# Kernel optimization log

Measured on AMD Instinct MI355X. Metric: run time of the kernel, lower is better.

## Reference

```python
import jax, jax.numpy as jnp
import numpy as np

FP4_VALUES = jnp.array([0.0, 0.5, 1.0, 1.5, 2.0, 3.0, 4.0, 6.0,
                        -0.0, -0.5, -1.0, -1.5, -2.0, -3.0, -4.0, -6.0], dtype=jnp.float32)
ALPHA = 1.702   # swiglu alpha
LIMIT = 7.0     # swiglu clamp limit
TOP_K = 4       # experts per token
EPS = 1e-5      # rmsnorm eps


def dequant_mxfp4(blocks, scales):
    """blocks: [E, R, G, B] int (uint8 values), scales: [E, R, G] int (E8M0 biased exp).
    Returns decoded weights [E, R, G*2B] fp32. Low nibble -> even cols, high nibble -> odd."""
    lo = FP4_VALUES[blocks & 15]
    hi = FP4_VALUES[(blocks >> 4) & 15]
    vals = jnp.stack([lo, hi], axis=-1).reshape(blocks.shape[:-1] + (-1,))  # [E,R,G,2B]
    w = jnp.ldexp(vals, (scales - 127)[..., None])
    return w.reshape(blocks.shape[:-2] + (-1,))


def rmsnorm(x, w):
    return x * jax.lax.rsqrt(jnp.mean(x * x, axis=-1, keepdims=True) + EPS) * w


def setup_inputs():
    key = jax.random.key(0)
    ks = jax.random.split(key, 10)
    E, H, I, B, S = 32, 1024, 1024, 1, 1024
    GB = 16  # packed bytes per 32-element group
    return {
        "x": jax.random.normal(ks[0], (B, S, H), jnp.float32),
        "norm_w": jnp.ones((H,), jnp.float32),
        "gate_w": jax.random.normal(ks[1], (E, H), jnp.float32) * 0.05,
        "gate_b": jax.random.normal(ks[2], (E,), jnp.float32) * 0.01,
        "mlp1_bias": jax.random.normal(ks[3], (E, 2 * I), jnp.float32) * 0.02,
        "mlp2_bias": jax.random.normal(ks[4], (E, H), jnp.float32) * 0.02,
        "mlp1_blocks": jax.random.randint(ks[5], (E, 2 * I, H // 32, GB), 0, 256, jnp.int32),
        "mlp1_scales": jax.random.randint(ks[6], (E, 2 * I, H // 32), 118, 125, jnp.int32),
        "mlp2_blocks": jax.random.randint(ks[7], (E, H, I // 32, GB), 0, 256, jnp.int32),
        "mlp2_scales": jax.random.randint(ks[8], (E, H, I // 32), 118, 125, jnp.int32),
    }


def reference(x, norm_w, gate_w, gate_b, mlp1_bias, mlp2_bias,
              mlp1_blocks, mlp1_scales, mlp2_blocks, mlp2_scales):
    B, S, H = x.shape
    N = B * S
    E = gate_w.shape[0]

    t = rmsnorm(x, norm_w).reshape(N, H)
    logits = t @ gate_w.T + gate_b                      # [N, E]
    top_vals, top_idx = jax.lax.top_k(logits, TOP_K)     # sorted descending, like torch.topk
    top_w = jax.nn.softmax(top_vals, axis=-1)            # [N, K]
    # dense routing matrix: nonzero only at selected experts (indices unique per token)
    route = jnp.zeros((N, E), x.dtype).at[jnp.arange(N)[:, None], top_idx].add(top_w)

    w1 = dequant_mxfp4(mlp1_blocks, mlp1_scales)         # [E, 2I, H]
    w2 = dequant_mxfp4(mlp2_blocks, mlp2_scales)         # [E, H, I]

    h = jnp.einsum('nh,eih->nei', t, w1) + mlp1_bias[None]  # [N, E, 2I]
    x_glu = jnp.minimum(h[..., 0::2], LIMIT)
    x_lin = jnp.clip(h[..., 1::2], -LIMIT, LIMIT)
    a = x_glu * jax.nn.sigmoid(ALPHA * x_glu) * (x_lin + 1.0)   # [N, E, I]
    y = jnp.einsum('nei,ehi->neh', a, w2) + mlp2_bias[None]      # [N, E, H]
    out = jnp.einsum('neh,ne->nh', y, route)                     # weighted combine
    return x + out.reshape(B, S, H)
```

## Files before the change

kernel.cpp:

```cpp
#include <hip/hip_runtime.h>
#include <hip/hip_bf16.h>
#include <math.h>


#define NE 32
#define HD 1024
#define ID 1024
#define NTOK 1024
#define R1 2048
#define TCH 160

typedef __attribute__((ext_vector_type(8)))  short bf16x8;
typedef __attribute__((ext_vector_type(16))) float f32x16;

#define TB_OFF   0
#define A_OFF    2097152
#define YB_OFF   10485760
#define CNT_OFF  18874368
#define OFFS_OFF 18874624
#define TOKL_OFF 18874880
#define TIDX_OFF 19005952
#define TWT_OFF  19022336
#define POS_OFF  19038720

__device__ __forceinline__ unsigned f2bf(float f) {
    unsigned u = __float_as_uint(f);
    return (u + 0x7FFFu + ((u >> 16) & 1u)) >> 16;
}
__device__ __forceinline__ float bf2f(unsigned u) {
    return __uint_as_float(u << 16);
}

__device__ __forceinline__ void dec8(int4 wv, unsigned dd, uint4& o) {
    unsigned u = __builtin_amdgcn_perm((unsigned)wv.y, (unsigned)wv.x, 0x00000400u);
    unsigned v = __builtin_amdgcn_perm((unsigned)wv.w, (unsigned)wv.z, 0x04000000u);
    unsigned packed = __builtin_amdgcn_perm(v, u, 0x07060100u);
    unsigned selE = packed & 0x07070707u;
    unsigned sE   = packed & 0x08080808u;
    unsigned ph   = packed >> 4;
    unsigned selO = ph & 0x07070707u;
    unsigned sO   = ph & 0x08080808u;
    const unsigned PH_hi = 0x40404040u, PH_lo = 0x3F3F3F14u;
    const unsigned PL_hi = 0xC0804000u, PL_lo = 0xC0800000u;
    unsigned hbE = __builtin_amdgcn_perm(PH_hi, PH_lo, selE) | (sE << 4);
    unsigned lbE = __builtin_amdgcn_perm(PL_hi, PL_lo, selE);
    unsigned hbO = __builtin_amdgcn_perm(PH_hi, PH_lo, selO) | (sO << 4);
    unsigned lbO = __builtin_amdgcn_perm(PL_hi, PL_lo, selO);
    unsigned mE0 = __builtin_amdgcn_perm(hbE, lbE, 0x05010400u);
    unsigned mE1 = __builtin_amdgcn_perm(hbE, lbE, 0x07030602u);
    unsigned mO0 = __builtin_amdgcn_perm(hbO, lbO, 0x05010400u);
    unsigned mO1 = __builtin_amdgcn_perm(hbO, lbO, 0x07030602u);
    unsigned r0 = __builtin_amdgcn_perm(mO0, mE0, 0x05040100u);
    unsigned r1 = __builtin_amdgcn_perm(mO0, mE0, 0x07060302u);
    unsigned r2 = __builtin_amdgcn_perm(mO1, mE1, 0x05040100u);
    unsigned r3 = __builtin_amdgcn_perm(mO1, mE1, 0x07060302u);
    unsigned o0, o1, o2, o3;
    asm("v_pk_add_u16 %0, %1, %2" : "=v"(o0) : "v"(r0), "v"(dd));
    asm("v_pk_add_u16 %0, %1, %2" : "=v"(o1) : "v"(r1), "v"(dd));
    asm("v_pk_add_u16 %0, %1, %2" : "=v"(o2) : "v"(r2), "v"(dd));
    asm("v_pk_add_u16 %0, %1, %2" : "=v"(o3) : "v"(r3), "v"(dd));
    o.x = o0; o.y = o1; o.z = o2; o.w = o3;
}

__global__ __launch_bounds__(256) void k_gate(
    const float* __restrict__ x, const float* __restrict__ norm_w,
    const float* __restrict__ gate_w, const float* __restrict__ gate_b,
    ushort* __restrict__ t_bf16, int* __restrict__ top_idx, float* __restrict__ top_wt)
{
    int n = blockIdx.x;
    int tid = threadIdx.x;
    __shared__ float tl[HD];
    __shared__ float red[4];
    __shared__ float logits[NE];

    const float4* xv = (const float4*)(x + (size_t)n * HD);
    float4 v = xv[tid];
    float ss = v.x * v.x + v.y * v.y + v.z * v.z + v.w * v.w;
    #pragma unroll
    for (int off = 32; off; off >>= 1) ss += __shfl_down(ss, off);
    if ((tid & 63) == 0) red[tid >> 6] = ss;
    __syncthreads();
    float tot = red[0] + red[1] + red[2] + red[3];
    float rms = rsqrtf(tot * (1.0f / HD) + 1e-5f);

    float4 w = ((const float4*)norm_w)[tid];
    float4 tv;
    tv.x = v.x * rms * w.x; tv.y = v.y * rms * w.y;
    tv.z = v.z * rms * w.z; tv.w = v.w * rms * w.w;
    ushort4 tb;
    tb.x = (ushort)f2bf(tv.x); tb.y = (ushort)f2bf(tv.y);
    tb.z = (ushort)f2bf(tv.z); tb.w = (ushort)f2bf(tv.w);
    ((ushort4*)(t_bf16 + (size_t)n * HD))[tid] = tb;
    ((float4*)tl)[tid] = tv;
    __syncthreads();

    int wv = tid >> 6, lane = tid & 63;
    for (int j = 0; j < 8; j++) {
        int e = wv * 8 + j;
        const float* gw = gate_w + (size_t)e * HD;
        float p = 0.f;
        #pragma unroll
        for (int q = 0; q < 16; q++) { int kk = lane + q * 64; p += tl[kk] * gw[kk]; }
        #pragma unroll
        for (int off = 32; off; off >>= 1) p += __shfl_down(p, off);
        if (lane == 0) logits[e] = p + gate_b[e];
    }
    __syncthreads();

    if (tid == 0) {
        float vals[4]; int idx[4];
        unsigned used = 0;
        #pragma unroll
        for (int kk = 0; kk < 4; kk++) {
            float best = -1e30f; int bi = 0;
            for (int e2 = 0; e2 < NE; e2++) {
                if (used & (1u << e2)) continue;
                if (logits[e2] > best) { best = logits[e2]; bi = e2; }
            }
            used |= 1u << bi; vals[kk] = best; idx[kk] = bi;
        }
        float m = vals[0], s = 0.f, ex[4];
        #pragma unroll
        for (int kk = 0; kk < 4; kk++) { ex[kk] = __expf(vals[kk] - m); s += ex[kk]; }
        float inv = 1.0f / s;
        #pragma unroll
        for (int kk = 0; kk < 4; kk++) {
            top_idx[n * 4 + kk] = idx[kk];
            top_wt[n * 4 + kk] = ex[kk] * inv;
        }
    }
}

__global__ void k_build(const int* __restrict__ top_idx, int* __restrict__ counts,
                        int* __restrict__ tok_list, int* __restrict__ pos_of)
{
    int i = blockIdx.x * 256 + threadIdx.x;
    if (i >= NTOK * 4) return;
    int n = i >> 2;
    int e = top_idx[i];
    int slot = atomicAdd(counts + e, 1);
    tok_list[e * NTOK + slot] = n;
    pos_of[i] = slot;
}

__global__ void k_prefix(const int* __restrict__ counts, int* __restrict__ offsets)
{
    if (threadIdx.x == 0) {
        int s = 0;
        for (int e = 0; e < NE; e++) { offsets[e] = s; s += counts[e]; }
        offsets[NE] = s;
    }
}

__global__ __launch_bounds__(256) void k_mlp1(
    const ushort* __restrict__ t_bf16, const int* __restrict__ blocks,
    const int* __restrict__ scales, const float* __restrict__ bias,
    const int* __restrict__ counts, const int* __restrict__ offsets,
    const int* __restrict__ tok_list, ushort* __restrict__ a)
{
    int e = blockIdx.y;
    int cnt = counts[e];
    if (cnt == 0) return;
    int r0 = blockIdx.x * 128;
    int tid = threadIdx.x;
    int w = tid >> 6, l = tid & 63;
    int base = offsets[e];

    __shared__ ushort tl[TCH][72];
    __shared__ ushort wl[128][72];
    __shared__ int tlist[TCH];

    int lrow = r0 + w * 32 + (l & 31);
    float b_lane = bias[e * R1 + lrow];
    int srow = tid >> 1, shalf = tid & 1;

    for (int c0 = 0; c0 < cnt; c0 += TCH) {
        int nt = min(TCH, cnt - c0);
        __syncthreads();
        if (tid < TCH) tlist[tid] = tok_list[e * NTOK + c0 + min(tid, nt - 1)];
        f32x16 acc[5] = {};

        #pragma unroll 1
        for (int k0 = 0; k0 < HD; k0 += 64) {
            __syncthreads();
            for (int idx = tid; idx < TCH * 8; idx += 256) {
                int tok = idx >> 3, seg = idx & 7;
                *(uint4*)&tl[tok][seg * 8] =
                    *(const uint4*)(t_bf16 + (size_t)tlist[tok] * HD + k0 + seg * 8);
            }
            {
                int g = (k0 >> 5) + shalf;
                size_t rbase = (size_t)(e * R1 + r0 + srow) * 32 + g;
                int s = scales[rbase];
                unsigned dd16 = (unsigned)((s - 127) << 7) & 0xFFFFu;
                unsigned dd = dd16 | (dd16 << 16);
                const int4* wp = (const int4*)(blocks + rbase * 16);
                ushort* dst = &wl[srow][shalf * 32];
                #pragma unroll
                for (int q = 0; q < 4; q++) {
                    uint4 ov;
                    dec8(wp[q], dd, ov);
                    *(uint4*)(dst + q * 8) = ov;
                }
            }
            __syncthreads();
            #pragma unroll
            for (int ks = 0; ks < 4; ks++) {
                bf16x8 wf = *(const bf16x8*)&wl[w * 32 + (l & 31)][ks * 16 + (l >> 5) * 8];
                #pragma unroll
                for (int mt = 0; mt < 5; mt++) {
                    bf16x8 af = *(const bf16x8*)&tl[mt * 32 + (l & 31)][ks * 16 + (l >> 5) * 8];
                    acc[mt] = __builtin_amdgcn_mfma_f32_32x32x16_bf16(af, wf, acc[mt], 0, 0, 0);
                }
            }
        }

        int p0 = (r0 + w * 32) >> 1;
        int pcol = p0 + ((l & 31) >> 1);
        #pragma unroll
        for (int mt = 0; mt < 5; mt++) {
            #pragma unroll
            for (int r = 0; r < 16; r++) {
                float h = acc[mt][r] + b_lane;
                float other = __shfl_xor(h, 1, 64);
                int m = (r & 3) + 8 * (r >> 2) + 4 * (l >> 5);
                int tokg = c0 + mt * 32 + m;
                if (!(l & 1) && tokg < cnt) {
                    float hg = fminf(h, 7.0f);
                    float hx = fminf(fmaxf(other, -7.0f), 7.0f);
                    float sig = 1.0f / (1.0f + __expf(-1.702f * hg));
                    float av = hg * sig * (hx + 1.0f);
                    a[(size_t)(base + tokg) * ID + pcol] = (ushort)f2bf(av);
                }
            }
        }
    }
}

__global__ __launch_bounds__(256) void k_mlp2(
    const ushort* __restrict__ a, const int* __restrict__ blocks,
    const int* __restrict__ scales, const float* __restrict__ bias,
    const int* __restrict__ counts, const int* __restrict__ offsets,
    ushort* __restrict__ yb)
{
    int e = blockIdx.y;
    int cnt = counts[e];
    if (cnt == 0) return;
    int r0 = blockIdx.x * 128;
    int tid = threadIdx.x;
    int w = tid >> 6, l = tid & 63;
    int base = offsets[e];

    __shared__ ushort tl[TCH][72];
    __shared__ ushort wl[128][72];

    int lrow = r0 + w * 32 + (l & 31);
    float b_lane = bias[e * HD + lrow];
    int srow = tid >> 1, shalf = tid & 1;

    for (int c0 = 0; c0 < cnt; c0 += TCH) {
        int nt = min(TCH, cnt - c0);
        f32x16 acc[5] = {};

        #pragma unroll 1
        for (int k0 = 0; k0 < ID; k0 += 64) {
            __syncthreads();
            for (int idx = tid; idx < TCH * 8; idx += 256) {
                int tok = idx >> 3, seg = idx & 7;
                int slot = base + c0 + min(tok, nt - 1);
                *(uint4*)&tl[tok][seg * 8] =
                    *(const uint4*)(a + (size_t)slot * ID + k0 + seg * 8);
            }
            {
                int g = (k0 >> 5) + shalf;
                size_t rbase = (size_t)(e * HD + r0 + srow) * 32 + g;
                int s = scales[rbase];
                unsigned dd16 = (unsigned)((s - 127) << 7) & 0xFFFFu;
                unsigned dd = dd16 | (dd16 << 16);
                const int4* wp = (const int4*)(blocks + rbase * 16);
                ushort* dst = &wl[srow][shalf * 32];
                #pragma unroll
                for (int q = 0; q < 4; q++) {
                    uint4 ov;
                    dec8(wp[q], dd, ov);
                    *(uint4*)(dst + q * 8) = ov;
                }
            }
            __syncthreads();
            #pragma unroll
            for (int ks = 0; ks < 4; ks++) {
                bf16x8 wf = *(const bf16x8*)&wl[w * 32 + (l & 31)][ks * 16 + (l >> 5) * 8];
                #pragma unroll
                for (int mt = 0; mt < 5; mt++) {
                    bf16x8 af = *(const bf16x8*)&tl[mt * 32 + (l & 31)][ks * 16 + (l >> 5) * 8];
                    acc[mt] = __builtin_amdgcn_mfma_f32_32x32x16_bf16(af, wf, acc[mt], 0, 0, 0);
                }
            }
        }

        int hcol = r0 + w * 32 + (l & 31);
        #pragma unroll
        for (int mt = 0; mt < 5; mt++) {
            #pragma unroll
            for (int r = 0; r < 16; r++) {
                int m = (r & 3) + 8 * (r >> 2) + 4 * (l >> 5);
                int tokg = c0 + mt * 32 + m;
                if (tokg < cnt) {
                    float y = acc[mt][r] + b_lane;
                    yb[(size_t)(base + tokg) * HD + hcol] = (ushort)f2bf(y);
                }
            }
        }
    }
}

__global__ __launch_bounds__(256) void k_combine(
    const float* __restrict__ x, const ushort* __restrict__ yb,
    const int* __restrict__ top_idx, const float* __restrict__ top_wt,
    const int* __restrict__ pos_of, const int* __restrict__ offsets,
    float* __restrict__ out)
{
    int n = blockIdx.x, tid = threadIdx.x;
    float4 xv = ((const float4*)(x + (size_t)n * HD))[tid];
    float r0 = xv.x, r1 = xv.y, r2 = xv.z, r3 = xv.w;
    #pragma unroll
    for (int k = 0; k < 4; k++) {
        int e = top_idx[n * 4 + k];
        float wt = top_wt[n * 4 + k];
        int slot = offsets[e] + pos_of[n * 4 + k];
        ushort4 yv = ((const ushort4*)(yb + (size_t)slot * HD))[tid];
        r0 += wt * bf2f(yv.x); r1 += wt * bf2f(yv.y);
        r2 += wt * bf2f(yv.z); r3 += wt * bf2f(yv.w);
    }
    float4 ov; ov.x = r0; ov.y = r1; ov.z = r2; ov.w = r3;
    ((float4*)(out + (size_t)n * HD))[tid] = ov;
}

extern "C" void kernel_launch(void* const* d_in, const int* in_sizes, int n_in,
                              void* d_out, int out_size, void* d_ws, size_t ws_size,
                              hipStream_t stream)
{
    const float* x           = (const float*)d_in[0];
    const float* norm_w      = (const float*)d_in[1];
    const float* gate_w      = (const float*)d_in[2];
    const float* gate_b      = (const float*)d_in[3];
    const float* mlp1_bias   = (const float*)d_in[4];
    const float* mlp2_bias   = (const float*)d_in[5];
    const int*   mlp1_blocks = (const int*)d_in[6];
    const int*   mlp1_scales = (const int*)d_in[7];
    const int*   mlp2_blocks = (const int*)d_in[8];
    const int*   mlp2_scales = (const int*)d_in[9];
    float* out = (float*)d_out;

    char* ws = (char*)d_ws;
    ushort* t_bf16  = (ushort*)(ws + TB_OFF);
    ushort* a       = (ushort*)(ws + A_OFF);
    ushort* yb      = (ushort*)(ws + YB_OFF);
    int*   counts   = (int*)(ws + CNT_OFF);
    int*   offsets  = (int*)(ws + OFFS_OFF);
    int*   tok_list = (int*)(ws + TOKL_OFF);
    int*   top_idx  = (int*)(ws + TIDX_OFF);
    float* top_wt   = (float*)(ws + TWT_OFF);
    int*   pos_of   = (int*)(ws + POS_OFF);

    hipMemsetAsync(counts, 0, NE * sizeof(int), stream);
    k_gate<<<NTOK, 256, 0, stream>>>(x, norm_w, gate_w, gate_b, t_bf16, top_idx, top_wt);
    k_build<<<(NTOK * 4 + 255) / 256, 256, 0, stream>>>(top_idx, counts, tok_list, pos_of);
    k_prefix<<<1, 64, 0, stream>>>(counts, offsets);
    k_mlp1<<<dim3(16, NE), 256, 0, stream>>>(t_bf16, mlp1_blocks, mlp1_scales, mlp1_bias,
                                             counts, offsets, tok_list, a);
    k_mlp2<<<dim3(8, NE), 256, 0, stream>>>(a, mlp2_blocks, mlp2_scales, mlp2_bias,
                                            counts, offsets, yb);
    k_combine<<<NTOK, 256, 0, stream>>>(x, yb, top_idx, top_wt, pos_of, offsets, out);
}
```

Baseline: 153.8 us.

## Decode MXFP4 weights into registers and double-buffer token tiles in MoE GEMMs

Rewrites both expert GEMM kernels so each lane decodes its own MXFP4 weight fragments directly into registers instead of staging decoded weights in shared memory. Token tiles are double-buffered in LDS, with the next tile's global loads issued before the MFMAs, and the warp tiling becomes 2x2 (64 rows by 96 tokens per wave). The token chunk size is raised from 160 to 192. Separately, the routing-list build is folded into the gate kernel, which removes one launch. The cost is higher register pressure and a custom barrier, in exchange for less LDS traffic and fewer syncs.

```diff
diff --git a/kernel.cpp b/kernel.cpp
--- a/kernel.cpp
+++ b/kernel.cpp
@@ -8,7 +8,7 @@
 #define ID 1024
 #define NTOK 1024
 #define R1 2048
-#define TCH 160
+#define TCH 192
 
 typedef __attribute__((ext_vector_type(8)))  short bf16x8;
 typedef __attribute__((ext_vector_type(16))) float f32x16;
@@ -31,7 +31,7 @@
     return __uint_as_float(u << 16);
 }
 
-__device__ __forceinline__ void dec8(int4 wv, unsigned dd, uint4& o) {
+__device__ __forceinline__ bf16x8 dec8(int4 wv, unsigned dd) {
     unsigned u = __builtin_amdgcn_perm((unsigned)wv.y, (unsigned)wv.x, 0x00000400u);
     unsigned v = __builtin_amdgcn_perm((unsigned)wv.w, (unsigned)wv.z, 0x04000000u);
     unsigned packed = __builtin_amdgcn_perm(v, u, 0x07060100u);
@@ -59,13 +59,23 @@
     asm("v_pk_add_u16 %0, %1, %2" : "=v"(o1) : "v"(r1), "v"(dd));
     asm("v_pk_add_u16 %0, %1, %2" : "=v"(o2) : "v"(r2), "v"(dd));
     asm("v_pk_add_u16 %0, %1, %2" : "=v"(o3) : "v"(r3), "v"(dd));
-    o.x = o0; o.y = o1; o.z = o2; o.w = o3;
+    uint4 o; o.x = o0; o.y = o1; o.z = o2; o.w = o3;
+    union { uint4 u4; bf16x8 b; } cv; cv.u4 = o;
+    return cv.b;
+}
+
+__device__ __forceinline__ void block_fence() {
+    asm volatile("s_waitcnt lgkmcnt(0)" ::: "memory");
+    __builtin_amdgcn_sched_barrier(0);
+    __builtin_amdgcn_s_barrier();
+    __builtin_amdgcn_sched_barrier(0);
 }
 
 __global__ __launch_bounds__(256) void k_gate(
     const float* __restrict__ x, const float* __restrict__ norm_w,
     const float* __restrict__ gate_w, const float* __restrict__ gate_b,
-    ushort* __restrict__ t_bf16, int* __restrict__ top_idx, float* __restrict__ top_wt)
+    ushort* __restrict__ t_bf16, int* __restrict__ top_idx, float* __restrict__ top_wt,
+    int* __restrict__ counts, int* __restrict__ tok_list, int* __restrict__ pos_of)
 {
     int n = blockIdx.x;
     int tid = threadIdx.x;
@@ -127,20 +137,11 @@
         for (int kk = 0; kk < 4; kk++) {
             top_idx[n * 4 + kk] = idx[kk];
             top_wt[n * 4 + kk] = ex[kk] * inv;
-        }
-    }
-}
-
-__global__ void k_build(const int* __restrict__ top_idx, int* __restrict__ counts,
-                        int* __restrict__ tok_list, int* __restrict__ pos_of)
-{
-    int i = blockIdx.x * 256 + threadIdx.x;
-    if (i >= NTOK * 4) return;
-    int n = i >> 2;
-    int e = top_idx[i];
-    int slot = atomicAdd(counts + e, 1);
-    tok_list[e * NTOK + slot] = n;
-    pos_of[i] = slot;
+            int slot = atomicAdd(counts + idx[kk], 1);
+            tok_list[idx[kk] * NTOK + slot] = n;
+            pos_of[n * 4 + kk] = slot;
+        }
+    }
 }
 
 __global__ void k_prefix(const int* __restrict__ counts, int* __restrict__ offsets)
@@ -164,73 +165,127 @@
     int r0 = blockIdx.x * 128;
     int tid = threadIdx.x;
     int w = tid >> 6, l = tid & 63;
+    int lr = l & 31, kh = l >> 5;
+    int nbase = (w & 1) * 64;
+    int tok0 = (w >> 1) * 96;
     int base = offsets[e];
 
-    __shared__ ushort tl[TCH][72];
-    __shared__ ushort wl[128][72];
-    __shared__ int tlist[TCH];
-
-    int lrow = r0 + w * 32 + (l & 31);
-    float b_lane = bias[e * R1 + lrow];
-    int srow = tid >> 1, shalf = tid & 1;
+    __shared__ ushort tl[2][TCH][72];
+
+    int nr0 = r0 + nbase + lr;
+    const int4* wp0 = (const int4*)blocks + (size_t)(e * R1 + nr0) * 128 + kh;
+    const int4* wp1 = wp0 + 32 * 128;
+    const int*  sp0 = scales + (size_t)(e * R1 + nr0) * 32;
+    const int*  sp1 = sp0 + 32 * 32;
+    float b0 = bias[e * R1 + nr0];
+    float b1 = bias[e * R1 + nr0 + 32];
+    int seg8 = (tid & 7) * 8;
 
     for (int c0 = 0; c0 < cnt; c0 += TCH) {
         int nt = min(TCH, cnt - c0);
-        __syncthreads();
-        if (tid < TCH) tlist[tid] = tok_list[e * NTOK + c0 + min(tid, nt - 1)];
-        f32x16 acc[5] = {};
+        int ntr = (nt + 31) & ~31;
+        int nmw = (nt - tok0 + 31) >> 5;
+        nmw = nmw < 0 ? 0 : (nmw > 3 ? 3 : nmw);
+
+        const ushort* tp[6]; bool act[6]; int trow[6];
+        #pragma unroll
+        for (int j = 0; j < 6; j++) {
+            int tok = (tid + j * 256) >> 3;
+            trow[j] = tok;
+            act[j] = tok < ntr;
+            int tok_c = tok < nt ? tok : nt - 1;
+            int n = tok_list[e * NTOK + c0 + tok_c];
+            tp[j] = t_bf16 + (size_t)n * HD + seg8;
+        }
+
+        int4 wb[2][4]; int2 sc[2];
+        sc[0] = *(const int2*)(sp0);
+        sc[1] = *(const int2*)(sp1);
+        #pragma unroll
+        for (int ks = 0; ks < 4; ks++) {
+            int off = (ks >> 1) * 4 + (ks & 1) * 2;
+            wb[0][ks] = wp0[off];
+            wb[1][ks] = wp1[off];
+        }
+        #pragma unroll
+        for (int j = 0; j < 6; j++) if (act[j]) {
+            uint4 tv = *(const uint4*)(tp[j]);
+            *(uint4*)&tl[0][trow[j]][seg8] = tv;
+        }
+        block_fence();
+
+        f32x16 acc[2][3] = {};
+        int cur = 0;
 
         #pragma unroll 1
-        for (int k0 = 0; k0 < HD; k0 += 64) {
-            __syncthreads();
-            for (int idx = tid; idx < TCH * 8; idx += 256) {
-                int tok = idx >> 3, seg = idx & 7;
-                *(uint4*)&tl[tok][seg * 8] =
-                    *(const uint4*)(t_bf16 + (size_t)tlist[tok] * HD + k0 + seg * 8);
-            }
-            {
-                int g = (k0 >> 5) + shalf;
-                size_t rbase = (size_t)(e * R1 + r0 + srow) * 32 + g;
-                int s = scales[rbase];
-                unsigned dd16 = (unsigned)((s - 127) << 7) & 0xFFFFu;
-                unsigned dd = dd16 | (dd16 << 16);
-                const int4* wp = (const int4*)(blocks + rbase * 16);
-                ushort* dst = &wl[srow][shalf * 32];
-                #pragma unroll
-                for (int q = 0; q < 4; q++) {
-                    uint4 ov;
-                    dec8(wp[q], dd, ov);
-                    *(uint4*)(dst + q * 8) = ov;
-                }
-            }
-            __syncthreads();
+        for (int kt = 0; kt < 16; kt++) {
+            bf16x8 wf[2][4];
+            #pragma unroll
+            for (int rr = 0; rr < 2; rr++) {
+                int sA = (rr ? sc[1].x : sc[0].x), sB = (rr ? sc[1].y : sc[0].y);
+                unsigned dA16 = (unsigned)((sA - 127) << 7) & 0xFFFFu;
+                unsigned dB16 = (unsigned)((sB - 127) << 7) & 0xFFFFu;
+                unsigned dA = dA16 | (dA16 << 16), dB = dB16 | (dB16 << 16);
+                wf[rr][0] = dec8(wb[rr][0], dA);
+                wf[rr][1] = dec8(wb[rr][1], dA);
+                wf[rr][2] = dec8(wb[rr][2], dB);
+                wf[rr][3] = dec8(wb[rr][3], dB);
+            }
+            uint4 tr[6];
+            if (kt < 15) {
+                int k1 = (kt + 1) * 64;
+                #pragma unroll
+                for (int j = 0; j < 6; j++) if (act[j]) tr[j] = *(const uint4*)(tp[j] + k1);
+                int g0 = (kt + 1) * 2;
+                sc[0] = *(const int2*)(sp0 + g0);
+                sc[1] = *(const int2*)(sp1 + g0);
+                #pragma unroll
+                for (int ks = 0; ks < 4; ks++) {
+                    int off = g0 * 4 + (ks >> 1) * 4 + (ks & 1) * 2;
+                    wb[0][ks] = wp0[off];
+                    wb[1][ks] = wp1[off];
+                }
+            }
             #pragma unroll
             for (int ks = 0; ks < 4; ks++) {
-                bf16x8 wf = *(const bf16x8*)&wl[w * 32 + (l & 31)][ks * 16 + (l >> 5) * 8];
-                #pragma unroll
-                for (int mt = 0; mt < 5; mt++) {
-                    bf16x8 af = *(const bf16x8*)&tl[mt * 32 + (l & 31)][ks * 16 + (l >> 5) * 8];
-                    acc[mt] = __builtin_amdgcn_mfma_f32_32x32x16_bf16(af, wf, acc[mt], 0, 0, 0);
-                }
-            }
-        }
-
-        int p0 = (r0 + w * 32) >> 1;
-        int pcol = p0 + ((l & 31) >> 1);
-        #pragma unroll
-        for (int mt = 0; mt < 5; mt++) {
-            #pragma unroll
-            for (int r = 0; r < 16; r++) {
-                float h = acc[mt][r] + b_lane;
-                float other = __shfl_xor(h, 1, 64);
-                int m = (r & 3) + 8 * (r >> 2) + 4 * (l >> 5);
-                int tokg = c0 + mt * 32 + m;
-                if (!(l & 1) && tokg < cnt) {
-                    float hg = fminf(h, 7.0f);
-                    float hx = fminf(fmaxf(other, -7.0f), 7.0f);
-                    float sig = 1.0f / (1.0f + __expf(-1.702f * hg));
-                    float av = hg * sig * (hx + 1.0f);
-                    a[(size_t)(base + tokg) * ID + pcol] = (ushort)f2bf(av);
+                #pragma unroll
+                for (int mt = 0; mt < 3; mt++) {
+                    if (mt < nmw) {
+                        bf16x8 af = *(const bf16x8*)&tl[cur][tok0 + mt * 32 + lr][ks * 16 + kh * 8];
+                        acc[0][mt] = __builtin_amdgcn_mfma_f32_32x32x16_bf16(af, wf[0][ks], acc[0][mt], 0, 0, 0);
+                        acc[1][mt] = __builtin_amdgcn_mfma_f32_32x32x16_bf16(af, wf[1][ks], acc[1][mt], 0, 0, 0);
+                    }
+                }
+            }
+            if (kt < 15) {
+                #pragma unroll
+                for (int j = 0; j < 6; j++) if (act[j])
+                    *(uint4*)&tl[cur ^ 1][trow[j]][seg8] = tr[j];
+            }
+            block_fence();
+            cur ^= 1;
+        }
+
+        #pragma unroll
+        for (int nn = 0; nn < 2; nn++) {
+            float bl = nn ? b1 : b0;
+            int col = r0 + nbase + nn * 32 + lr;
+            int pcol = col >> 1;
+            #pragma unroll
+            for (int mt = 0; mt < 3; mt++) {
+                #pragma unroll
+                for (int r = 0; r < 16; r++) {
+                    float h = acc[nn][mt][r] + bl;
+                    float other = __shfl_xor(h, 1, 64);
+                    int m = (r & 3) + 8 * (r >> 2) + 4 * kh;
+                    int tokg = c0 + tok0 + mt * 32 + m;
+                    if (!(l & 1) && tokg < cnt) {
+                        float hg = fminf(h, 7.0f);
+                        float hx = fminf(fmaxf(other, -7.0f), 7.0f);
+                        float sig = 1.0f / (1.0f + __expf(-1.702f * hg));
+                        float av = hg * sig * (hx + 1.0f);
+                        a[(size_t)(base + tokg) * ID + pcol] = (ushort)f2bf(av);
+                    }
                 }
             }
         }
@@ -249,65 +304,120 @@
     int r0 = blockIdx.x * 128;
     int tid = threadIdx.x;
     int w = tid >> 6, l = tid & 63;
+    int lr = l & 31, kh = l >> 5;
+    int nbase = (w & 1) * 64;
+    int tok0 = (w >> 1) * 96;
     int base = offsets[e];
 
-    __shared__ ushort tl[TCH][72];
-    __shared__ ushort wl[128][72];
-
-    int lrow = r0 + w * 32 + (l & 31);
-    float b_lane = bias[e * HD + lrow];
-    int srow = tid >> 1, shalf = tid & 1;
+    __shared__ ushort tl[2][TCH][72];
+
+    int nr0 = r0 + nbase + lr;
+    const int4* wp0 = (const int4*)blocks + (size_t)(e * HD + nr0) * 128 + kh;
+    const int4* wp1 = wp0 + 32 * 128;
+    const int*  sp0 = scales + (size_t)(e * HD + nr0) * 32;
+    const int*  sp1 = sp0 + 32 * 32;
+    float b0 = bias[e * HD + nr0];
+    float b1 = bias[e * HD + nr0 + 32];
+    int seg8 = (tid & 7) * 8;
 
     for (int c0 = 0; c0 < cnt; c0 += TCH) {
         int nt = min(TCH, cnt - c0);
-        f32x16 acc[5] = {};
+        int ntr = (nt + 31) & ~31;
+        int nmw = (nt - tok0 + 31) >> 5;
+        nmw = nmw < 0 ? 0 : (nmw > 3 ? 3 : nmw);
+
+        const ushort* tp[6]; bool act[6]; int trow[6];
+        #pragma unroll
+        for (int j = 0; j < 6; j++) {
+            int tok = (tid + j * 256) >> 3;
+            trow[j] = tok;
+            act[j] = tok < ntr;
+            int tok_c = tok < nt ? tok : nt - 1;
+            tp[j] = a + (size_t)(base + c0 + tok_c) * ID + seg8;
+        }
+
+        int4 wb[2][4]; int2 sc[2];
+        sc[0] = *(const int2*)(sp0);
+        sc[1] = *(const int2*)(sp1);
+        #pragma unroll
+        for (int ks = 0; ks < 4; ks++) {
+            int off = (ks >> 1) * 4 + (ks & 1) * 2;
+            wb[0][ks] = wp0[off];
+            wb[1][ks] = wp1[off];
+        }
+        #pragma unroll
+        for (int j = 0; j < 6; j++) if (act[j]) {
+            uint4 tv = *(const uint4*)(tp[j]);
+            *(uint4*)&tl[0][trow[j]][seg8] = tv;
+        }
+        block_fence();
+
+        f32x16 acc[2][3] = {};
+        int cur = 0;
 
         #pragma unroll 1
-        for (int k0 = 0; k0 < ID; k0 += 64) {
-            __syncthreads();
-            for (int idx = tid; idx < TCH * 8; idx += 256) {
-                int tok = idx >> 3, seg = idx & 7;
-                int slot = base + c0 + min(tok, nt - 1);
-                *(uint4*)&tl[tok][seg * 8] =
-                    *(const uint4*)(a + (size_t)slot * ID + k0 + seg * 8);
-            }
-            {
-                int g = (k0 >> 5) + shalf;
-                size_t rbase = (size_t)(e * HD + r0 + srow) * 32 + g;
-                int s = scales[rbase];
-                unsigned dd16 = (unsigned)((s - 127) << 7) & 0xFFFFu;
-                unsigned dd = dd16 | (dd16 << 16);
-                const int4* wp = (const int4*)(blocks + rbase * 16);
-                ushort* dst = &wl[srow][shalf * 32];
-                #pragma unroll
-                for (int q = 0; q < 4; q++) {
-                    uint4 ov;
-                    dec8(wp[q], dd, ov);
-                    *(uint4*)(dst + q * 8) = ov;
-                }
-            }
-            __syncthreads();
+        for (int kt = 0; kt < 16; kt++) {
+            bf16x8 wf[2][4];
+            #pragma unroll
+            for (int rr = 0; rr < 2; rr++) {
+                int sA = (rr ? sc[1].x : sc[0].x), sB = (rr ? sc[1].y : sc[0].y);
+                unsigned dA16 = (unsigned)((sA - 127) << 7) & 0xFFFFu;
+                unsigned dB16 = (unsigned)((sB - 127) << 7) & 0xFFFFu;
+                unsigned dA = dA16 | (dA16 << 16), dB = dB16 | (dB16 << 16);
+                wf[rr][0] = dec8(wb[rr][0], dA);
+                wf[rr][1] = dec8(wb[rr][1], dA);
+                wf[rr][2] = dec8(wb[rr][2], dB);
+                wf[rr][3] = dec8(wb[rr][3], dB);
+            }
+            uint4 tr[6];
+            if (kt < 15) {
+                int k1 = (kt + 1) * 64;
+                #pragma unroll
+                for (int j = 0; j < 6; j++) if (act[j]) tr[j] = *(const uint4*)(tp[j] + k1);
+                int g0 = (kt + 1) * 2;
+                sc[0] = *(const int2*)(sp0 + g0);
+                sc[1] = *(const int2*)(sp1 + g0);
+                #pragma unroll
+                for (int ks = 0; ks < 4; ks++) {
+                    int off = g0 * 4 + (ks >> 1) * 4 + (ks & 1) * 2;
+                    wb[0][ks] = wp0[off];
+                    wb[1][ks] = wp1[off];
+                }
+            }
             #pragma unroll
             for (int ks = 0; ks < 4; ks++) {
-                bf16x8 wf = *(const bf16x8*)&wl[w * 32 + (l & 31)][ks * 16 + (l >> 5) * 8];
-                #pragma unroll
-                for (int mt = 0; mt < 5; mt++) {
-                    bf16x8 af = *(const bf16x8*)&tl[mt * 32 + (l & 31)][ks * 16 + (l >> 5) * 8];
-                    acc[mt] = __builtin_amdgcn_mfma_f32_32x32x16_bf16(af, wf, acc[mt], 0, 0, 0);
-                }
-            }
-        }
-
-        int hcol = r0 + w * 32 + (l & 31);
-        #pragma unroll
-        for (int mt = 0; mt < 5; mt++) {
-            #pragma unroll
-            for (int r = 0; r < 16; r++) {
-                int m = (r & 3) + 8 * (r >> 2) + 4 * (l >> 5);
-                int tokg = c0 + mt * 32 + m;
-                if (tokg < cnt) {
-                    float y = acc[mt][r] + b_lane;
-                    yb[(size_t)(base + tokg) * HD + hcol] = (ushort)f2bf(y);
+                #pragma unroll
+                for (int mt = 0; mt < 3; mt++) {
+                    if (mt < nmw) {
+                        bf16x8 af = *(const bf16x8*)&tl[cur][tok0 + mt * 32 + lr][ks * 16 + kh * 8];
+                        acc[0][mt] = __builtin_amdgcn_mfma_f32_32x32x16_bf16(af, wf[0][ks], acc[0][mt], 0, 0, 0);
+                        acc[1][mt] = __builtin_amdgcn_mfma_f32_32x32x16_bf16(af, wf[1][ks], acc[1][mt], 0, 0, 0);
+                    }
+                }
+            }
+            if (kt < 15) {
+                #pragma unroll
+                for (int j = 0; j < 6; j++) if (act[j])
+                    *(uint4*)&tl[cur ^ 1][trow[j]][seg8] = tr[j];
+            }
+            block_fence();
+            cur ^= 1;
+        }
+
+        #pragma unroll
+        for (int nn = 0; nn < 2; nn++) {
+            float bl = nn ? b1 : b0;
+            int col = r0 + nbase + nn * 32 + lr;
+            #pragma unroll
+            for (int mt = 0; mt < 3; mt++) {
+                #pragma unroll
+                for (int r = 0; r < 16; r++) {
+                    int m = (r & 3) + 8 * (r >> 2) + 4 * kh;
+                    int tokg = c0 + tok0 + mt * 32 + m;
+                    if (tokg < cnt) {
+                        float y = acc[nn][mt][r] + bl;
+                        yb[(size_t)(base + tokg) * HD + col] = (ushort)f2bf(y);
+                    }
                 }
             }
         }
@@ -364,8 +474,8 @@
     int*   pos_of   = (int*)(ws + POS_OFF);
 
     hipMemsetAsync(counts, 0, NE * sizeof(int), stream);
-    k_gate<<<NTOK, 256, 0, stream>>>(x, norm_w, gate_w, gate_b, t_bf16, top_idx, top_wt);
-    k_build<<<(NTOK * 4 + 255) / 256, 256, 0, stream>>>(top_idx, counts, tok_list, pos_of);
+    k_gate<<<NTOK, 256, 0, stream>>>(x, norm_w, gate_w, gate_b, t_bf16, top_idx, top_wt,
+                                     counts, tok_list, pos_of);
     k_prefix<<<1, 64, 0, stream>>>(counts, offsets);
     k_mlp1<<<dim3(16, NE), 256, 0, stream>>>(t_bf16, mlp1_blocks, mlp1_scales, mlp1_bias,
                                              counts, offsets, tok_list, a);
```

New measurement: 249.3 us. 1.62x slower.

## Decode MXFP4 weights in registers, double-buffer token tiles, split tokens across z-grid

Applied to the files above, without the earlier changes.

The MLP kernels now decode FP4 weights straight into MFMA register fragments instead of staging them in LDS, and use a double-buffered LDS token tile with register prefetch of the next K-step's weights and activations. Tokens are split into 64-token chunks spread over a third grid dimension (4 z-blocks), which raises block count and occupancy. The routing-list build is folded into the gate kernel, removing one launch. The cost is that each weight row is re-read and re-decoded by every z-block that has tokens, and register pressure goes up from the prefetch buffers.

```diff
diff --git a/kernel.cpp b/kernel.cpp
--- a/kernel.cpp
+++ b/kernel.cpp
@@ -8,7 +8,6 @@
 #define ID 1024
 #define NTOK 1024
 #define R1 2048
-#define TCH 160
 
 typedef __attribute__((ext_vector_type(8)))  short bf16x8;
 typedef __attribute__((ext_vector_type(16))) float f32x16;
@@ -31,7 +30,7 @@
     return __uint_as_float(u << 16);
 }
 
-__device__ __forceinline__ void dec8(int4 wv, unsigned dd, uint4& o) {
+__device__ __forceinline__ bf16x8 dec8(int4 wv, unsigned dd) {
     unsigned u = __builtin_amdgcn_perm((unsigned)wv.y, (unsigned)wv.x, 0x00000400u);
     unsigned v = __builtin_amdgcn_perm((unsigned)wv.w, (unsigned)wv.z, 0x04000000u);
     unsigned packed = __builtin_amdgcn_perm(v, u, 0x07060100u);
@@ -59,13 +58,23 @@
     asm("v_pk_add_u16 %0, %1, %2" : "=v"(o1) : "v"(r1), "v"(dd));
     asm("v_pk_add_u16 %0, %1, %2" : "=v"(o2) : "v"(r2), "v"(dd));
     asm("v_pk_add_u16 %0, %1, %2" : "=v"(o3) : "v"(r3), "v"(dd));
-    o.x = o0; o.y = o1; o.z = o2; o.w = o3;
+    uint4 o; o.x = o0; o.y = o1; o.z = o2; o.w = o3;
+    union { uint4 u4; bf16x8 b; } cv; cv.u4 = o;
+    return cv.b;
+}
+
+__device__ __forceinline__ void fence_lds() {
+    asm volatile("s_waitcnt lgkmcnt(0)" ::: "memory");
+    __builtin_amdgcn_sched_barrier(0);
+    __builtin_amdgcn_s_barrier();
+    __builtin_amdgcn_sched_barrier(0);
 }
 
 __global__ __launch_bounds__(256) void k_gate(
     const float* __restrict__ x, const float* __restrict__ norm_w,
     const float* __restrict__ gate_w, const float* __restrict__ gate_b,
-    ushort* __restrict__ t_bf16, int* __restrict__ top_idx, float* __restrict__ top_wt)
+    ushort* __restrict__ t_bf16, int* __restrict__ top_idx, float* __restrict__ top_wt,
+    int* __restrict__ counts, int* __restrict__ tok_list, int* __restrict__ pos_of)
 {
     int n = blockIdx.x;
     int tid = threadIdx.x;
@@ -127,20 +136,11 @@
         for (int kk = 0; kk < 4; kk++) {
             top_idx[n * 4 + kk] = idx[kk];
             top_wt[n * 4 + kk] = ex[kk] * inv;
-        }
-    }
-}
-
-__global__ void k_build(const int* __restrict__ top_idx, int* __restrict__ counts,
-                        int* __restrict__ tok_list, int* __restrict__ pos_of)
-{
-    int i = blockIdx.x * 256 + threadIdx.x;
-    if (i >= NTOK * 4) return;
-    int n = i >> 2;
-    int e = top_idx[i];
-    int slot = atomicAdd(counts + e, 1);
-    tok_list[e * NTOK + slot] = n;
-    pos_of[i] = slot;
+            int slot = atomicAdd(counts + idx[kk], 1);
+            tok_list[idx[kk] * NTOK + slot] = n;
+            pos_of[n * 4 + kk] = slot;
+        }
+    }
 }
 
 __global__ void k_prefix(const int* __restrict__ counts, int* __restrict__ offsets)
@@ -160,77 +160,108 @@
 {
     int e = blockIdx.y;
     int cnt = counts[e];
-    if (cnt == 0) return;
     int r0 = blockIdx.x * 128;
     int tid = threadIdx.x;
-    int w = tid >> 6, l = tid & 63;
+    int l = tid & 63;
+    int lr = l & 31, kh = l >> 5;
     int base = offsets[e];
 
-    __shared__ ushort tl[TCH][72];
-    __shared__ ushort wl[128][72];
-    __shared__ int tlist[TCH];
-
-    int lrow = r0 + w * 32 + (l & 31);
-    float b_lane = bias[e * R1 + lrow];
-    int srow = tid >> 1, shalf = tid & 1;
-
-    for (int c0 = 0; c0 < cnt; c0 += TCH) {
-        int nt = min(TCH, cnt - c0);
-        __syncthreads();
-        if (tid < TCH) tlist[tid] = tok_list[e * NTOK + c0 + min(tid, nt - 1)];
-        f32x16 acc[5] = {};
+    __shared__ ushort tl[2][64][72];
+
+    int row = r0 + (tid >> 6) * 32 + lr;
+    const int4* wp = (const int4*)blocks + (size_t)(e * R1 + row) * 128 + kh;
+    const int*  sp = scales + (size_t)(e * R1 + row) * 32;
+    float bl = bias[e * R1 + row];
+    int srow = tid & 63;
+    int scol0 = (tid >> 6) * 8;
+    int scol1 = scol0 + 32;
+
+    for (int c0 = blockIdx.z * 64; c0 < cnt; c0 += 256) {
+        int nt = min(64, cnt - c0);
+        int nmt = (nt + 31) >> 5;
+        const ushort* tp = t_bf16 + (size_t)tok_list[e * NTOK + c0 + min(srow, nt - 1)] * HD;
+
+        uint4 t0a = *(const uint4*)(tp + scol0);
+        uint4 t0b = *(const uint4*)(tp + scol1);
+        int4 wbA[4], wbB[4]; int2 scA, scB;
+        #pragma unroll
+        for (int ks = 0; ks < 4; ks++) wbA[ks] = wp[2 * ks];
+        scA = *(const int2*)sp;
+        #pragma unroll
+        for (int ks = 0; ks < 4; ks++) wbB[ks] = wp[8 + 2 * ks];
+        scB = *(const int2*)(sp + 2);
+        uint4 tra = *(const uint4*)(tp + 64 + scol0);
+        uint4 trb = *(const uint4*)(tp + 64 + scol1);
+        *(uint4*)&tl[0][srow][scol0] = t0a;
+        *(uint4*)&tl[0][srow][scol1] = t0b;
+        fence_lds();
+
+        f32x16 acc[2] = {};
 
         #pragma unroll 1
-        for (int k0 = 0; k0 < HD; k0 += 64) {
-            __syncthreads();
-            for (int idx = tid; idx < TCH * 8; idx += 256) {
-                int tok = idx >> 3, seg = idx & 7;
-                *(uint4*)&tl[tok][seg * 8] =
-                    *(const uint4*)(t_bf16 + (size_t)tlist[tok] * HD + k0 + seg * 8);
+        for (int kt2 = 0; kt2 < 16; kt2 += 2) {
+            #pragma unroll
+            for (int h = 0; h < 2; h++) {
+                int kt = kt2 + h;
+                int sA = h ? scB.x : scA.x;
+                int sB = h ? scB.y : scA.y;
+                unsigned dA16 = (unsigned)((sA - 127) << 7) & 0xFFFFu;
+                unsigned dB16 = (unsigned)((sB - 127) << 7) & 0xFFFFu;
+                unsigned dA = dA16 | (dA16 << 16), dB = dB16 | (dB16 << 16);
+                bf16x8 wf0 = dec8(h ? wbB[0] : wbA[0], dA);
+                bf16x8 wf1 = dec8(h ? wbB[1] : wbA[1], dA);
+                bf16x8 wf2 = dec8(h ? wbB[2] : wbA[2], dB);
+                bf16x8 wf3 = dec8(h ? wbB[3] : wbA[3], dB);
+                if (kt < 15) {
+                    *(uint4*)&tl[h ^ 1][srow][scol0] = tra;
+                    *(uint4*)&tl[h ^ 1][srow][scol1] = trb;
+                }
+                if (kt < 14) {
+                    const ushort* tpk = tp + (kt + 2) * 64;
+                    tra = *(const uint4*)(tpk + scol0);
+                    trb = *(const uint4*)(tpk + scol1);
+                    int woff = (kt + 2) * 8;
+                    if (h) {
+                        #pragma unroll
+                        for (int ks = 0; ks < 4; ks++) wbB[ks] = wp[woff + 2 * ks];
+                        scB = *(const int2*)(sp + (kt + 2) * 2);
+                    } else {
+                        #pragma unroll
+                        for (int ks = 0; ks < 4; ks++) wbA[ks] = wp[woff + 2 * ks];
+                        scA = *(const int2*)(sp + (kt + 2) * 2);
+                    }
+                }
+                #pragma unroll
+                for (int mt = 0; mt < 2; mt++) {
+                    if (mt < nmt) {
+                        bf16x8 af0 = *(const bf16x8*)&tl[h][mt * 32 + lr][kh * 8];
+                        acc[mt] = __builtin_amdgcn_mfma_f32_32x32x16_bf16(af0, wf0, acc[mt], 0, 0, 0);
+                        bf16x8 af1 = *(const bf16x8*)&tl[h][mt * 32 + lr][16 + kh * 8];
+                        acc[mt] = __builtin_amdgcn_mfma_f32_32x32x16_bf16(af1, wf1, acc[mt], 0, 0, 0);
+                        bf16x8 af2 = *(const bf16x8*)&tl[h][mt * 32 + lr][32 + kh * 8];
+                        acc[mt] = __builtin_amdgcn_mfma_f32_32x32x16_bf16(af2, wf2, acc[mt], 0, 0, 0);
+                        bf16x8 af3 = *(const bf16x8*)&tl[h][mt * 32 + lr][48 + kh * 8];
+                        acc[mt] = __builtin_amdgcn_mfma_f32_32x32x16_bf16(af3, wf3, acc[mt], 0, 0, 0);
+                    }
+                }
+                fence_lds();
             }
-            {
-                int g = (k0 >> 5) + shalf;
-                size_t rbase = (size_t)(e * R1 + r0 + srow) * 32 + g;
-                int s = scales[rbase];
-                unsigned dd16 = (unsigned)((s - 127) << 7) & 0xFFFFu;
-                unsigned dd = dd16 | (dd16 << 16);
-                const int4* wp = (const int4*)(blocks + rbase * 16);
-                ushort* dst = &wl[srow][shalf * 32];
-                #pragma unroll
-                for (int q = 0; q < 4; q++) {
-                    uint4 ov;
-                    dec8(wp[q], dd, ov);
-                    *(uint4*)(dst + q * 8) = ov;
-                }
-            }
-            __syncthreads();
-            #pragma unroll
-            for (int ks = 0; ks < 4; ks++) {
-                bf16x8 wf = *(const bf16x8*)&wl[w * 32 + (l & 31)][ks * 16 + (l >> 5) * 8];
-                #pragma unroll
-                for (int mt = 0; mt < 5; mt++) {
-                    bf16x8 af = *(const bf16x8*)&tl[mt * 32 + (l & 31)][ks * 16 + (l >> 5) * 8];
-                    acc[mt] = __builtin_amdgcn_mfma_f32_32x32x16_bf16(af, wf, acc[mt], 0, 0, 0);
-                }
-            }
-        }
-
-        int p0 = (r0 + w * 32) >> 1;
-        int pcol = p0 + ((l & 31) >> 1);
-        #pragma unroll
-        for (int mt = 0; mt < 5; mt++) {
+        }
+
+        #pragma unroll
+        for (int mt = 0; mt < 2; mt++) {
             #pragma unroll
             for (int r = 0; r < 16; r++) {
-                float h = acc[mt][r] + b_lane;
-                float other = __shfl_xor(h, 1, 64);
-                int m = (r & 3) + 8 * (r >> 2) + 4 * (l >> 5);
+                float hv = acc[mt][r] + bl;
+                float other = __shfl_xor(hv, 1, 64);
+                int m = (r & 3) + 8 * (r >> 2) + 4 * kh;
                 int tokg = c0 + mt * 32 + m;
                 if (!(l & 1) && tokg < cnt) {
-                    float hg = fminf(h, 7.0f);
+                    float hg = fminf(hv, 7.0f);
                     float hx = fminf(fmaxf(other, -7.0f), 7.0f);
                     float sig = 1.0f / (1.0f + __expf(-1.702f * hg));
                     float av = hg * sig * (hx + 1.0f);
-                    a[(size_t)(base + tokg) * ID + pcol] = (ushort)f2bf(av);
+                    a[(size_t)(base + tokg) * ID + (row >> 1)] = (ushort)f2bf(av);
                 }
             }
         }
@@ -245,69 +276,103 @@
 {
     int e = blockIdx.y;
     int cnt = counts[e];
-    if (cnt == 0) return;
     int r0 = blockIdx.x * 128;
     int tid = threadIdx.x;
-    int w = tid >> 6, l = tid & 63;
+    int l = tid & 63;
+    int lr = l & 31, kh = l >> 5;
     int base = offsets[e];
 
-    __shared__ ushort tl[TCH][72];
-    __shared__ ushort wl[128][72];
-
-    int lrow = r0 + w * 32 + (l & 31);
-    float b_lane = bias[e * HD + lrow];
-    int srow = tid >> 1, shalf = tid & 1;
-
-    for (int c0 = 0; c0 < cnt; c0 += TCH) {
-        int nt = min(TCH, cnt - c0);
-        f32x16 acc[5] = {};
+    __shared__ ushort tl[2][64][72];
+
+    int row = r0 + (tid >> 6) * 32 + lr;
+    const int4* wp = (const int4*)blocks + (size_t)(e * HD + row) * 128 + kh;
+    const int*  sp = scales + (size_t)(e * HD + row) * 32;
+    float bl = bias[e * HD + row];
+    int srow = tid & 63;
+    int scol0 = (tid >> 6) * 8;
+    int scol1 = scol0 + 32;
+
+    for (int c0 = blockIdx.z * 64; c0 < cnt; c0 += 256) {
+        int nt = min(64, cnt - c0);
+        int nmt = (nt + 31) >> 5;
+        const ushort* tp = a + (size_t)(base + c0 + min(srow, nt - 1)) * ID;
+
+        uint4 t0a = *(const uint4*)(tp + scol0);
+        uint4 t0b = *(const uint4*)(tp + scol1);
+        int4 wbA[4], wbB[4]; int2 scA, scB;
+        #pragma unroll
+        for (int ks = 0; ks < 4; ks++) wbA[ks] = wp[2 * ks];
+        scA = *(const int2*)sp;
+        #pragma unroll
+        for (int ks = 0; ks < 4; ks++) wbB[ks] = wp[8 + 2 * ks];
+        scB = *(const int2*)(sp + 2);
+        uint4 tra = *(const uint4*)(tp + 64 + scol0);
+        uint4 trb = *(const uint4*)(tp + 64 + scol1);
+        *(uint4*)&tl[0][srow][scol0] = t0a;
+        *(uint4*)&tl[0][srow][scol1] = t0b;
+        fence_lds();
+
+        f32x16 acc[2] = {};
 
         #pragma unroll 1
-        for (int k0 = 0; k0 < ID; k0 += 64) {
-            __syncthreads();
-            for (int idx = tid; idx < TCH * 8; idx += 256) {
-                int tok = idx >> 3, seg = idx & 7;
-                int slot = base + c0 + min(tok, nt - 1);
-                *(uint4*)&tl[tok][seg * 8] =
-                    *(const uint4*)(a + (size_t)slot * ID + k0 + seg * 8);
+        for (int kt2 = 0; kt2 < 16; kt2 += 2) {
+            #pragma unroll
+            for (int h = 0; h < 2; h++) {
+                int kt = kt2 + h;
+                int sA = h ? scB.x : scA.x;
+                int sB = h ? scB.y : scA.y;
+                unsigned dA16 = (unsigned)((sA - 127) << 7) & 0xFFFFu;
+                unsigned dB16 = (unsigned)((sB - 127) << 7) & 0xFFFFu;
+                unsigned dA = dA16 | (dA16 << 16), dB = dB16 | (dB16 << 16);
+                bf16x8 wf0 = dec8(h ? wbB[0] : wbA[0], dA);
+                bf16x8 wf1 = dec8(h ? wbB[1] : wbA[1], dA);
+                bf16x8 wf2 = dec8(h ? wbB[2] : wbA[2], dB);
+                bf16x8 wf3 = dec8(h ? wbB[3] : wbA[3], dB);
+                if (kt < 15) {
+                    *(uint4*)&tl[h ^ 1][srow][scol0] = tra;
+                    *(uint4*)&tl[h ^ 1][srow][scol1] = trb;
+                }
+                if (kt < 14) {
+                    const ushort* tpk = tp + (kt + 2) * 64;
+                    tra = *(const uint4*)(tpk + scol0);
+                    trb = *(const uint4*)(tpk + scol1);
+                    int woff = (kt + 2) * 8;
+                    if (h) {
+                        #pragma unroll
+                        for (int ks = 0; ks < 4; ks++) wbB[ks] = wp[woff + 2 * ks];
+                        scB = *(const int2*)(sp + (kt + 2) * 2);
+                    } else {
+                        #pragma unroll
+                        for (int ks = 0; ks < 4; ks++) wbA[ks] = wp[woff + 2 * ks];
+                        scA = *(const int2*)(sp + (kt + 2) * 2);
+                    }
+                }
+                #pragma unroll
+                for (int mt = 0; mt < 2; mt++) {
+                    if (mt < nmt) {
+                        bf16x8 af0 = *(const bf16x8*)&tl[h][mt * 32 + lr][kh * 8];
+                        acc[mt] = __builtin_amdgcn_mfma_f32_32x32x16_bf16(af0, wf0, acc[mt], 0, 0, 0);
+                        bf16x8 af1 = *(const bf16x8*)&tl[h][mt * 32 + lr][16 + kh * 8];
+                        acc[mt] = __builtin_amdgcn_mfma_f32_32x32x16_bf16(af1, wf1, acc[mt], 0, 0, 0);
+                        bf16x8 af2 = *(const bf16x8*)&tl[h][mt * 32 + lr][32 + kh * 8];
+                        acc[mt] = __builtin_amdgcn_mfma_f32_32x32x16_bf16(af2, wf2, acc[mt], 0, 0, 0);
+                        bf16x8 af3 = *(const bf16x8*)&tl[h][mt * 32 + lr][48 + kh * 8];
+                        acc[mt] = __builtin_amdgcn_mfma_f32_32x32x16_bf16(af3, wf3, acc[mt], 0, 0, 0);
+                    }
+                }
+                fence_lds();
             }
-            {
-                int g = (k0 >> 5) + shalf;
-                size_t rbase = (size_t)(e * HD + r0 + srow) * 32 + g;
-                int s = scales[rbase];
-                unsigned dd16 = (unsigned)((s - 127) << 7) & 0xFFFFu;
-                unsigned dd = dd16 | (dd16 << 16);
-                const int4* wp = (const int4*)(blocks + rbase * 16);
-                ushort* dst = &wl[srow][shalf * 32];
-                #pragma unroll
-                for (int q = 0; q < 4; q++) {
-                    uint4 ov;
-                    dec8(wp[q], dd, ov);
-                    *(uint4*)(dst + q * 8) = ov;
-                }
-            }
-            __syncthreads();
-            #pragma unroll
-            for (int ks = 0; ks < 4; ks++) {
-                bf16x8 wf = *(const bf16x8*)&wl[w * 32 + (l & 31)][ks * 16 + (l >> 5) * 8];
-                #pragma unroll
-                for (int mt = 0; mt < 5; mt++) {
-                    bf16x8 af = *(const bf16x8*)&tl[mt * 32 + (l & 31)][ks * 16 + (l >> 5) * 8];
-                    acc[mt] = __builtin_amdgcn_mfma_f32_32x32x16_bf16(af, wf, acc[mt], 0, 0, 0);
-                }
-            }
-        }
-
-        int hcol = r0 + w * 32 + (l & 31);
-        #pragma unroll
-        for (int mt = 0; mt < 5; mt++) {
+        }
+
+        #pragma unroll
+        for (int mt = 0; mt < 2; mt++) {
             #pragma unroll
             for (int r = 0; r < 16; r++) {
-                int m = (r & 3) + 8 * (r >> 2) + 4 * (l >> 5);
+                int m = (r & 3) + 8 * (r >> 2) + 4 * kh;
                 int tokg = c0 + mt * 32 + m;
                 if (tokg < cnt) {
-                    float y = acc[mt][r] + b_lane;
-                    yb[(size_t)(base + tokg) * HD + hcol] = (ushort)f2bf(y);
+                    float y = acc[mt][r] + bl;
+                    yb[(size_t)(base + tokg) * HD + row] = (ushort)f2bf(y);
                 }
             }
         }
@@ -364,12 +429,12 @@
     int*   pos_of   = (int*)(ws + POS_OFF);
 
     hipMemsetAsync(counts, 0, NE * sizeof(int), stream);
-    k_gate<<<NTOK, 256, 0, stream>>>(x, norm_w, gate_w, gate_b, t_bf16, top_idx, top_wt);
-    k_build<<<(NTOK * 4 + 255) / 256, 256, 0, stream>>>(top_idx, counts, tok_list, pos_of);
+    k_gate<<<NTOK, 256, 0, stream>>>(x, norm_w, gate_w, gate_b, t_bf16, top_idx, top_wt,
+                                     counts, tok_list, pos_of);
     k_prefix<<<1, 64, 0, stream>>>(counts, offsets);
-    k_mlp1<<<dim3(16, NE), 256, 0, stream>>>(t_bf16, mlp1_blocks, mlp1_scales, mlp1_bias,
-                                             counts, offsets, tok_list, a);
-    k_mlp2<<<dim3(8, NE), 256, 0, stream>>>(a, mlp2_blocks, mlp2_scales, mlp2_bias,
-                                            counts, offsets, yb);
+    k_mlp1<<<dim3(16, NE, 4), 256, 0, stream>>>(t_bf16, mlp1_blocks, mlp1_scales, mlp1_bias,
+                                                counts, offsets, tok_list, a);
+    k_mlp2<<<dim3(8, NE, 4), 256, 0, stream>>>(a, mlp2_blocks, mlp2_scales, mlp2_bias,
+                                               counts, offsets, yb);
     k_combine<<<NTOK, 256, 0, stream>>>(x, yb, top_idx, top_wt, pos_of, offsets, out);
 }
```

Result: slower. 191.5 us (+24.5%).
